# Performance work log

Measured on AMD Instinct MI355X. Metric: run time of the kernel, lower is better.

The kernel has to match this reference:

```python
import math
import jax, jax.numpy as jnp
import numpy as np

H = 768      # hidden_size
NH = 12      # num_attention_heads
K = 3        # attention_num branches (wid = None, 2, 4)
DIV = 5.0    # gauss_divisor = 2**(attention_num-1) + 1
SFT = 1.0    # sft_factor
WIDTHS = (None, 2.0, 4.0)
B, L = 4, 1024


def _layernorm(x, s, b, eps=1e-5):
    m = jnp.mean(x, axis=-1, keepdims=True)
    v = jnp.mean((x - m) ** 2, axis=-1, keepdims=True)
    return (x - m) / jnp.sqrt(v + eps) * s + b


def _log_gauss_bias(props_len, width):
    # matches generate_gauss_weight + log(clamp_min(1e-6))
    center = jnp.arange(props_len, dtype=jnp.float32) / props_len          # (L,)
    wt = jnp.maximum(jnp.float32(width), 0.01) / DIV                       # scalar
    pos = jnp.linspace(0.0, 1.0, props_len)                                # (L,)
    g = (0.3989422804014327 / wt) * jnp.exp(-(pos[None, :] - center[:, None]) ** 2 / (2.0 * wt * wt))
    g = g / jnp.max(g, axis=-1, keepdims=True)
    return jnp.log(jnp.maximum(g, 1e-6))                                   # (L, L)


def _attn(qx, kx, vx, Wq, bq, Wk, bk, Wv, bv, bias, mask):
    Bn, Lq, D = qx.shape
    dh = D // NH
    q = (qx @ Wq + bq).reshape(Bn, Lq, NH, dh)
    k = (kx @ Wk + bk).reshape(Bn, kx.shape[1], NH, dh)
    v = (vx @ Wv + bv).reshape(Bn, vx.shape[1], NH, dh)
    s = jnp.einsum('bqhd,bkhd->bhqk', q, k) / math.sqrt(dh)
    if bias is not None:
        s = s + bias[None, None]                  # cached Gaussian log-bias
    if mask is not None:
        s = s + (1.0 - mask)[:, None, None, :] * (-10000.0)
    p = jax.nn.softmax(s, axis=-1)
    return jnp.einsum('bhqk,bkhd->bqhd', p, v).reshape(Bn, Lq, D)


def _block(x, mask, Wq, bq, Wk, bk, Wv, bv, W1, b1, W2, b2, n1s, n1b, n2s, n2b, bias):
    a = _attn(x, x, x, Wq, bq, Wk, bk, Wv, bv, bias, mask)
    x = _layernorm(x + a, n1s, n1b)
    h = jax.nn.relu(x @ W1 + b1) @ W2 + b2
    return _layernorm(x + h, n2s, n2b)


def setup_inputs():
    key = jax.random.key(0)
    ks = iter(jax.random.split(key, 64))
    def p(*sh):
        return jax.random.normal(next(ks), sh, dtype=jnp.float32) * 0.02
    inp = {}
    inp['input_tensor'] = jax.random.normal(next(ks), (B, L, H), dtype=jnp.float32)
    inp['attention_mask'] = jnp.ones((B, L), dtype=jnp.float32)
    for nm, sh in [('bWq', (K, H, H)), ('bWk', (K, H, H)), ('bWv', (K, H, H)),
                   ('bW1', (K, H, 4 * H)), ('bW2', (K, 4 * H, H)),
                   ('caWq', (H, H)), ('caWk', (H, H)), ('caWv', (H, H)),
                   ('caW1', (H, H)), ('caW2', (H, H)), ('Wl1', (H, H)), ('Wl2', (H, 1))]:
        inp[nm] = p(*sh)
    for nm, sh in [('bbq', (K, H)), ('bbk', (K, H)), ('bbv', (K, H)), ('bb1', (K, 4 * H)), ('bb2', (K, H)),
                   ('cabq', (H,)), ('cabk', (H,)), ('cabv', (H,)), ('cab1', (H,)), ('cab2', (H,)),
                   ('bl1', (H,)), ('bl2', (1,))]:
        inp[nm] = jnp.zeros(sh, dtype=jnp.float32)
    for nm, sh in [('bn1s', (K, H)), ('bn2s', (K, H)), ('bns', (H,)), ('can1s', (H,)), ('can2s', (H,))]:
        inp[nm] = jnp.ones(sh, dtype=jnp.float32)
    for nm, sh in [('bn1b', (K, H)), ('bn2b', (K, H)), ('bnb', (H,)), ('can1b', (H,)), ('can2b', (H,))]:
        inp[nm] = jnp.zeros(sh, dtype=jnp.float32)
    return inp


def reference(input_tensor, attention_mask, bWq, bbq, bWk, bbk, bWv, bbv, bW1, bb1, bW2, bb2,
              bn1s, bn1b, bn2s, bn2b, bns, bnb,
              caWq, cabq, caWk, cabk, caWv, cabv, caW1, cab1, caW2, cab2,
              can1s, can1b, can2s, can2b, Wl1, bl1, Wl2, bl2):
    Bn, Ln, _ = input_tensor.shape
    mask = attention_mask
    biases = [None if w is None else _log_gauss_bias(Ln, w) for w in WIDTHS]
    outs = []
    for i in range(K):
        o = _block(input_tensor, mask,
                   bWq[i], bbq[i], bWk[i], bbk[i], bWv[i], bbv[i],
                   bW1[i], bb1[i], bW2[i], bb2[i],
                   bn1s[i], bn1b[i], bn2s[i], bn2b[i], biases[i])
        outs.append(_layernorm(o, bns, bnb))
    oo = jnp.stack(outs, axis=-1)                                   # (B, L, H, K)
    valid = mask                                                    # (B, L)
    denom = jnp.maximum(valid.sum(axis=1, keepdims=True), 1.0)      # (B, 1)
    mean_token = (oo.mean(-1) * valid[:, :, None]).sum(axis=1, keepdims=True) / denom[:, :, None]  # (B,1,H)
    selected = mean_token  # weight_token=None, mode='global' -> global_token = mean_token
    branch_feat = jnp.transpose(oo, (0, 3, 1, 2)).reshape(Bn * K, Ln, H)
    query_token = jnp.repeat(selected, K, axis=0)                   # (B*K, 1, H)
    branch_mask = jnp.repeat(mask, K, axis=0)                       # (B*K, L)
    # CrossAttention (wid=None, FFN d_ff = H)
    a = _attn(query_token, branch_feat, branch_feat, caWq, cabq, caWk, cabk, caWv, cabv, None, branch_mask)
    q = _layernorm(query_token + a, can1s, can1b)
    t = jax.nn.relu(q @ caW1 + cab1) @ caW2 + cab2
    q = _layernorm(q + t, can2s, can2b)                             # (B*K, 1, H)
    w = q.reshape(Bn, K, H)
    w = jax.nn.relu(w @ Wl1 + bl1)
    w = (w @ Wl2 + bl2)[..., 0]                                     # (B, K)
    w = jax.nn.softmax(w / SFT, axis=-1)
    return (oo * w[:, None, None, :]).sum(axis=-1)                  # (B, L, H)
```

## Files before the change

### kernel.cpp

```cpp
#include <hip/hip_runtime.h>
#include <hip/hip_bf16.h>
#include <cstdint>
#include <cmath>

typedef __hip_bfloat16 bf16;
typedef __attribute__((ext_vector_type(8))) __bf16 bf16x8;
typedef __attribute__((ext_vector_type(4))) float f32x4;

#define NE2C ((size_t)4096 * 768)

__device__ inline float ldv(const void* __restrict__ p, size_t i, bool b){
  return b ? __bfloat162float(((const bf16*)p)[i]) : ((const float*)p)[i];
}

__device__ inline float wave_sum(float v){
  #pragma unroll
  for (int o = 1; o < 64; o <<= 1) v += __shfl_xor(v, o, 64);
  return v;
}
__device__ inline float wave_max(float v){
  #pragma unroll
  for (int o = 1; o < 64; o <<= 1) v = fmaxf(v, __shfl_xor(v, o, 64));
  return v;
}

__device__ __forceinline__ void gload_lds16(const __bf16* g, __bf16* l){
  __builtin_amdgcn_global_load_lds(
      (const __attribute__((address_space(1))) uint32_t*)g,
      (__attribute__((address_space(3))) uint32_t*)l,
      16, 0, 0);
}

__global__ void flag_kernel(const void* __restrict__ bns, int* __restrict__ flagp){
  if (threadIdx.x == 0) flagp[0] = (((const uint32_t*)bns)[0] == 0x3F800000u) ? 0 : 1;
}

__global__ __launch_bounds__(256) void cvtb_kernel(const void* __restrict__ in, __bf16* __restrict__ out,
                                                   int n, const int* __restrict__ flagp){
  const bool isb = flagp[0] != 0;
  int i = blockIdx.x * 256 + threadIdx.x;
  if (i < n) out[i] = (__bf16)ldv(in, i, isb);
}

__global__ __launch_bounds__(256) void transpose_kernel(const void* __restrict__ in, size_t in_off, size_t in_zstride,
    __bf16* __restrict__ out, size_t out_off, size_t out_zstride, int K, int N, const int* __restrict__ flagp)
{
  const bool isb = flagp[0] != 0;
  const int z = blockIdx.z;
  const size_t ioff = in_off + (size_t)z * in_zstride;
  __bf16* op = out + out_off + (size_t)z * out_zstride;
  const int n0 = blockIdx.x * 64, k0 = blockIdx.y * 64;
  __shared__ __bf16 T[64][65];
  const int cr = threadIdx.x >> 6, cc = threadIdx.x & 63;
  #pragma unroll
  for (int it = 0; it < 16; ++it) {
    int r = it * 4 + cr;
    T[r][cc] = (__bf16)ldv(in, ioff + (size_t)(k0 + r) * N + (n0 + cc), isb);
  }
  __syncthreads();
  #pragma unroll
  for (int it = 0; it < 16; ++it) {
    int r = it * 4 + cr;
    op[(size_t)(n0 + r) * K + (k0 + cc)] = T[cc][r];
  }
}

__global__ __launch_bounds__(256) void biaspack_kernel(const void* bbq, const void* bbk, const void* bbv,
    const void* bb1, const void* bb2, const void* cabk, const void* cabv,
    float* __restrict__ pool, const int* __restrict__ flagp)
{
  const bool isb = flagp[0] != 0;
  int idx = blockIdx.x * 256 + threadIdx.x;
  if (idx >= 19968) return;
  float v;
  if (idx < 6912) {
    int i = idx / 2304, rem = idx % 2304;
    int m = rem / 768, c = rem % 768;
    const void* src = (m == 0) ? bbq : ((m == 1) ? bbk : bbv);
    v = ldv(src, (size_t)i * 768 + c, isb);
  } else if (idx < 16128) v = ldv(bb1, idx - 6912, isb);
  else if (idx < 18432)   v = ldv(bb2, idx - 16128, isb);
  else if (idx < 19200)   v = ldv(cabk, idx - 18432, isb);
  else                    v = ldv(cabv, idx - 19200, isb);
  pool[idx] = v;
}

__global__ __launch_bounds__(256) void gaussbias_kernel(float* __restrict__ gb)
{
  const int br = blockIdx.x >> 10;
  const int q  = blockIdx.x & 1023;
  const float inv2wt2 = (br == 0) ? 3.125f : 0.78125f;
  const float c2 = inv2wt2 * 1.4426950408889634f;
  const float cq = (float)q * (1.f / 1024.f);
  const float kst = roundf(cq * 1023.f);
  const float dd = kst * (1.f / 1023.f) - cq;
  const float dmin = dd * dd;
  float* row = gb + (size_t)br * 1048576 + (size_t)q * 1024;
  for (int j = threadIdx.x; j < 1024; j += 256) {
    float d2 = (float)j * (1.f / 1023.f) - cq;
    row[j] = fmaxf((dmin - d2 * d2) * c2, -19.9315686f);
  }
}

__global__ __launch_bounds__(256) void gemm_mfma_kernel(
    const __bf16* __restrict__ A, size_t a_zstride,
    const __bf16* __restrict__ WT, const float* __restrict__ biasp,
    __bf16* __restrict__ C, int M, int N, int K, int relu)
{
  const int z = blockIdx.z;
  A  += (size_t)z * a_zstride;
  WT += (size_t)z * (size_t)N * K;
  biasp += (size_t)z * N;
  C  += (size_t)z * (size_t)M * N;
  const int m0 = blockIdx.y * 128, n0 = blockIdx.x * 128;
  const int tid = threadIdx.x, w = tid >> 6, lane = tid & 63;
  const int quad = lane >> 4, r16 = lane & 15;
  const int wr = w >> 1, wc = w & 1;
  __shared__ __align__(16) __bf16 As[128 * 32];
  __shared__ __align__(16) __bf16 Bs[128 * 32];
  f32x4 acc[4][4];
  #pragma unroll
  for (int i = 0; i < 4; ++i)
    #pragma unroll
    for (int j = 0; j < 4; ++j) acc[i][j] = (f32x4){0.f, 0.f, 0.f, 0.f};

  const int srow = tid >> 2;
  const int scc  = (tid & 3) * 8;

  for (int k0 = 0; k0 < K; k0 += 32) {
    __syncthreads();
    #pragma unroll
    for (int it = 0; it < 2; ++it) {
      int row = it * 64 + srow;
      const __bf16* gA = A  + (size_t)(m0 + row) * K + k0 + scc;
      const __bf16* gB = WT + (size_t)(n0 + row) * K + k0 + scc;
      __bf16* lA = &As[(it * 256 + w * 64) * 8];
      __bf16* lB = &Bs[(it * 256 + w * 64) * 8];
      gload_lds16(gA, lA);
      gload_lds16(gB, lB);
    }
    __syncthreads();
    bf16x8 af[4], bf[4];
    #pragma unroll
    for (int mt = 0; mt < 4; ++mt) af[mt] = *(const bf16x8*)&As[(wr * 64 + mt * 16 + r16) * 32 + quad * 8];
    #pragma unroll
    for (int nt = 0; nt < 4; ++nt) bf[nt] = *(const bf16x8*)&Bs[(wc * 64 + nt * 16 + r16) * 32 + quad * 8];
    #pragma unroll
    for (int mt = 0; mt < 4; ++mt)
      #pragma unroll
      for (int nt = 0; nt < 4; ++nt)
        acc[mt][nt] = __builtin_amdgcn_mfma_f32_16x16x32_bf16(af[mt], bf[nt], acc[mt][nt], 0, 0, 0);
  }
  #pragma unroll
  for (int nt = 0; nt < 4; ++nt) {
    int col = n0 + wc * 64 + nt * 16 + r16;
    float bv = biasp[col];
    #pragma unroll
    for (int mt = 0; mt < 4; ++mt) {
      int rowb = m0 + wr * 64 + mt * 16 + quad * 4;
      #pragma unroll
      for (int reg = 0; reg < 4; ++reg) {
        float v = acc[mt][nt][reg] + bv;
        if (relu) v = fmaxf(v, 0.f);
        C[(size_t)(rowb + reg) * N + col] = (__bf16)v;
      }
    }
  }
}

__global__ __launch_bounds__(256) void gemm_small_kernel(const float* __restrict__ A, const void* __restrict__ W,
    size_t woff, const void* __restrict__ bias, size_t boff, float* __restrict__ C,
    int N, int K, int relu, const int* __restrict__ flagp)
{
  const bool isb = flagp[0] != 0;
  const int row = blockIdx.y;
  const int c = blockIdx.x * 64 + (threadIdx.x & 63);
  const int ks = threadIdx.x >> 6;
  const int klen = K >> 2;
  const float* ar = A + (size_t)row * K + ks * klen;
  const size_t wbase = woff + (size_t)ks * klen * N + c;
  float acc = 0.f;
  #pragma unroll 4
  for (int k = 0; k < klen; ++k)
    acc += ar[k] * ldv(W, wbase + (size_t)k * N, isb);
  __shared__ float red[4][64];
  red[ks][threadIdx.x & 63] = acc;
  __syncthreads();
  if (threadIdx.x < 64) {
    float v = red[0][threadIdx.x] + red[1][threadIdx.x] + red[2][threadIdx.x] + red[3][threadIdx.x];
    v += ldv(bias, boff + c, isb);
    if (relu) v = fmaxf(v, 0.f);
    C[(size_t)row * N + c] = v;
  }
}

__global__ __launch_bounds__(256) void attn_mfma_kernel(
    const __bf16* __restrict__ QKV, const void* __restrict__ mask,
    const float* __restrict__ gbias,
    __bf16* __restrict__ Aout, const int* __restrict__ flagp)
{
  const bool isb = flagp[0] != 0;
  const int bz = blockIdx.z;
  const int b = bz & 3, br = bz >> 2;
  const __bf16* Q  = QKV + (size_t)br * 3 * NE2C;
  const __bf16* Kg = Q + NE2C;
  const __bf16* Vg = Q + 2 * NE2C;
  Aout += (size_t)br * NE2C;
  const int has_bias = br > 0;

  const int h = blockIdx.y;
  const int tid = threadIdx.x;
  const int w = tid >> 6, lane = tid & 63;
  const int quad = lane >> 4, r16 = lane & 15;
  const int qbase = blockIdx.x * 64 + w * 16;

  __shared__ __align__(16) __bf16 Ks[64 * 72];
  __shared__ __align__(16) __bf16 Vt[64 * 72];
  __shared__ __align__(16) __bf16 Ps[4][16 * 72];

  const __bf16* qrow = Q + ((size_t)(b * 1024 + qbase + r16)) * 768 + h * 64;
  bf16x8 aq0 = *(const bf16x8*)(qrow + quad * 8);
  bf16x8 aq1 = *(const bf16x8*)(qrow + 32 + quad * 8);

  const float* brow[4];
  if (has_bias) {
    const float* gb = gbias + (size_t)(br - 1) * 1048576 + r16;
    #pragma unroll
    for (int reg = 0; reg < 4; ++reg)
      brow[reg] = gb + (size_t)(qbase + quad * 4 + reg) * 1024;
  }

  float m_r[4], l_r[4];
  f32x4 O[4];
  #pragma unroll
  for (int n = 0; n < 4; ++n) O[n] = (f32x4){0.f, 0.f, 0.f, 0.f};
  #pragma unroll
  for (int reg = 0; reg < 4; ++reg) { m_r[reg] = -1e30f; l_r[reg] = 0.f; }

  const int dd = tid & 63;
  const int rb = tid >> 6;
  const int dswz = (dd >> 3) & 7;

  const int kr_row0 = tid >> 3;
  const int kr_c8   = (tid & 7) * 8;
  const size_t kcol  = (size_t)h * 64 + kr_c8;
  const size_t vcol  = (size_t)h * 64 + dd;
  const size_t bbase = (size_t)b * 1024;

  const float SCL = 0.18033688f;
  const float MBIG = 14426.9504f;
  const float THR2 = 11.5415603f;

  bf16x8 kpre0, kpre1;
  bf16x8 vpre0, vpre1;

  {
    kpre0 = *(const bf16x8*)(Kg + (bbase + kr_row0)      * 768 + kcol);
    kpre1 = *(const bf16x8*)(Kg + (bbase + kr_row0 + 32) * 768 + kcol);
    const int r0 = rb * 16;
    #pragma unroll
    for (int i = 0; i < 8; ++i) {
      vpre0[i] = Vg[(bbase + r0 + i)     * 768 + vcol];
      vpre1[i] = Vg[(bbase + r0 + 8 + i) * 768 + vcol];
    }
  }

  for (int c0 = 0; c0 < 1024; c0 += 64) {
    __syncthreads();
    *(bf16x8*)&Ks[kr_row0 * 72 + kr_c8]        = kpre0;
    *(bf16x8*)&Ks[(kr_row0 + 32) * 72 + kr_c8] = kpre1;
    {
      int blk0 = ((rb * 16)     >> 3) ^ dswz;
      int blk1 = ((rb * 16 + 8) >> 3) ^ dswz;
      *(bf16x8*)&Vt[dd * 72 + blk0 * 8] = vpre0;
      *(bf16x8*)&Vt[dd * 72 + blk1 * 8] = vpre1;
    }
    __syncthreads();

    if (c0 + 64 < 1024) {
      const size_t cb = bbase + c0 + 64;
      kpre0 = *(const bf16x8*)(Kg + (cb + kr_row0)      * 768 + kcol);
      kpre1 = *(const bf16x8*)(Kg + (cb + kr_row0 + 32) * 768 + kcol);
      const int r0 = rb * 16;
      #pragma unroll
      for (int i = 0; i < 8; ++i) {
        vpre0[i] = Vg[(cb + r0 + i)     * 768 + vcol];
        vpre1[i] = Vg[(cb + r0 + 8 + i) * 768 + vcol];
      }
    }

    float s4[4][4], p4[4][4];
    #pragma unroll
    for (int t = 0; t < 4; ++t) {
      bf16x8 b0 = *(const bf16x8*)&Ks[(t * 16 + r16) * 72 + quad * 8];
      bf16x8 b1 = *(const bf16x8*)&Ks[(t * 16 + r16) * 72 + 32 + quad * 8];
      f32x4 accq = (f32x4){0.f, 0.f, 0.f, 0.f};
      accq = __builtin_amdgcn_mfma_f32_16x16x32_bf16(aq0, b0, accq, 0, 0, 0);
      accq = __builtin_amdgcn_mfma_f32_16x16x32_bf16(aq1, b1, accq, 0, 0, 0);
      int kk = c0 + t * 16 + r16;
      float mk = ldv(mask, (size_t)(b * 1024 + kk), isb);
      float mterm = fmaf(mk, MBIG, -MBIG);
      if (has_bias) {
        #pragma unroll
        for (int reg = 0; reg < 4; ++reg)
          s4[t][reg] = fmaf(accq[reg], SCL, mterm) + brow[reg][c0 + t * 16];
      } else {
        #pragma unroll
        for (int reg = 0; reg < 4; ++reg)
          s4[t][reg] = fmaf(accq[reg], SCL, mterm);
      }
    }
    float tm[4];
    #pragma unroll
    for (int reg = 0; reg < 4; ++reg) {
      float t0 = fmaxf(fmaxf(s4[0][reg], s4[1][reg]), fmaxf(s4[2][reg], s4[3][reg]));
      #pragma unroll
      for (int off = 1; off < 16; off <<= 1) t0 = fmaxf(t0, __shfl_xor(t0, off, 64));
      tm[reg] = t0;
    }
    bool nosc = (tm[0] - m_r[0] <= THR2) && (tm[1] - m_r[1] <= THR2)
             && (tm[2] - m_r[2] <= THR2) && (tm[3] - m_r[3] <= THR2);
    if (!__all(nosc)) {
      #pragma unroll
      for (int reg = 0; reg < 4; ++reg) {
        float mnew = fmaxf(m_r[reg], tm[reg]);
        float alpha = exp2f(m_r[reg] - mnew);
        l_r[reg] *= alpha;
        m_r[reg] = mnew;
        #pragma unroll
        for (int n = 0; n < 4; ++n) O[n][reg] *= alpha;
      }
    }
    #pragma unroll
    for (int reg = 0; reg < 4; ++reg) {
      float rs = 0.f;
      #pragma unroll
      for (int t = 0; t < 4; ++t) { float p = exp2f(s4[t][reg] - m_r[reg]); p4[t][reg] = p; rs += p; }
      l_r[reg] += rs;
    }
    __bf16* pw = &Ps[w][0];
    #pragma unroll
    for (int t = 0; t < 4; ++t)
      #pragma unroll
      for (int reg = 0; reg < 4; ++reg)
        pw[(quad * 4 + reg) * 72 + t * 16 + r16] = (__bf16)p4[t][reg];
    bf16x8 ap0 = *(const bf16x8*)&pw[r16 * 72 + quad * 8];
    bf16x8 ap1 = *(const bf16x8*)&pw[r16 * 72 + 32 + quad * 8];
    __builtin_amdgcn_s_setprio(1);
    #pragma unroll
    for (int n = 0; n < 4; ++n) {
      int dr = n * 16 + r16;
      int sw = (dr >> 3) & 7;
      bf16x8 bv0 = *(const bf16x8*)&Vt[dr * 72 + (quad ^ sw) * 8];
      bf16x8 bv1 = *(const bf16x8*)&Vt[dr * 72 + ((quad + 4) ^ sw) * 8];
      O[n] = __builtin_amdgcn_mfma_f32_16x16x32_bf16(ap0, bv0, O[n], 0, 0, 0);
      O[n] = __builtin_amdgcn_mfma_f32_16x16x32_bf16(ap1, bv1, O[n], 0, 0, 0);
    }
    __builtin_amdgcn_s_setprio(0);
  }
  #pragma unroll
  for (int reg = 0; reg < 4; ++reg) {
    float lv = l_r[reg];
    #pragma unroll
    for (int off = 1; off < 16; off <<= 1) lv += __shfl_xor(lv, off, 64);
    l_r[reg] = lv;
  }
  #pragma unroll
  for (int n = 0; n < 4; ++n)
    #pragma unroll
    for (int reg = 0; reg < 4; ++reg) {
      int qg = qbase + quad * 4 + reg;
      Aout[((size_t)(b * 1024 + qg)) * 768 + h * 64 + n * 16 + r16] = (__bf16)(O[n][reg] / l_r[reg]);
    }
}

__global__ __launch_bounds__(256) void lnb_b_kernel(const __bf16* __restrict__ x, const __bf16* __restrict__ a,
    const void* __restrict__ sc, const void* __restrict__ bi, __bf16* __restrict__ out,
    const int* __restrict__ flagp)
{
  const bool isb = flagp[0] != 0;
  const int br = blockIdx.y;
  a   += (size_t)br * NE2C;
  out += (size_t)br * NE2C;
  const size_t so = (size_t)br * 768;
  int r = blockIdx.x;
  const __bf16* xr = x + (size_t)r * 768;
  const __bf16* ar = a + (size_t)r * 768;
  int t = threadIdx.x;
  float v[3]; float s = 0.f, ss = 0.f;
  #pragma unroll
  for (int j = 0; j < 3; j++) {
    int c = t + j * 256;
    float val = (float)xr[c] + (float)ar[c];
    v[j] = val; s += val; ss += val * val;
  }
  s = wave_sum(s); ss = wave_sum(ss);
  __shared__ float sred[8];
  __shared__ float stats[2];
  int lane = t & 63, wid = t >> 6;
  if (lane == 0) { sred[wid] = s; sred[4 + wid] = ss; }
  __syncthreads();
  if (t == 0) {
    float S = sred[0] + sred[1] + sred[2] + sred[3];
    float SS = sred[4] + sred[5] + sred[6] + sred[7];
    float mean = S * (1.f / 768.f);
    float var = fmaxf(SS * (1.f / 768.f) - mean * mean, 0.f);
    stats[0] = mean; stats[1] = rsqrtf(var + 1e-5f);
  }
  __syncthreads();
  float mean = stats[0], rstd = stats[1];
  #pragma unroll
  for (int j = 0; j < 3; j++) {
    int c = t + j * 256;
    out[(size_t)r * 768 + c] = (__bf16)((v[j] - mean) * rstd * ldv(sc, so + c, isb) + ldv(bi, so + c, isb));
  }
}

__global__ __launch_bounds__(256) void lnb2_b_kernel(const __bf16* __restrict__ x, const __bf16* __restrict__ a,
    const void* __restrict__ sc1, const void* __restrict__ bi1,
    const void* __restrict__ sc2, const void* __restrict__ bi2,
    __bf16* __restrict__ out, const int* __restrict__ flagp)
{
  const bool isb = flagp[0] != 0;
  const int br = blockIdx.y;
  x   += (size_t)br * NE2C;
  a   += (size_t)br * NE2C;
  out += (size_t)br * NE2C;
  const size_t s1off = (size_t)br * 768;
  int r = blockIdx.x;
  const __bf16* xr = x + (size_t)r * 768;
  const __bf16* ar = a + (size_t)r * 768;
  int t = threadIdx.x;
  int lane = t & 63, wid = t >> 6;
  __shared__ float sred[8], stats[2], sred2[8], stats2[2];

  float v[3]; float s = 0.f, ss = 0.f;
  #pragma unroll
  for (int j = 0; j < 3; j++) {
    int c = t + j * 256;
    float val = (float)xr[c] + (float)ar[c];
    v[j] = val; s += val; ss += val * val;
  }
  s = wave_sum(s); ss = wave_sum(ss);
  if (lane == 0) { sred[wid] = s; sred[4 + wid] = ss; }
  __syncthreads();
  if (t == 0) {
    float S = sred[0] + sred[1] + sred[2] + sred[3];
    float SS = sred[4] + sred[5] + sred[6] + sred[7];
    float mean = S * (1.f / 768.f);
    float var = fmaxf(SS * (1.f / 768.f) - mean * mean, 0.f);
    stats[0] = mean; stats[1] = rsqrtf(var + 1e-5f);
  }
  __syncthreads();
  float mean = stats[0], rstd = stats[1];
  float y[3]; float s2 = 0.f, ss2 = 0.f;
  #pragma unroll
  for (int j = 0; j < 3; j++) {
    int c = t + j * 256;
    float yv = (v[j] - mean) * rstd * ldv(sc1, s1off + c, isb) + ldv(bi1, s1off + c, isb);
    yv = (float)(__bf16)yv;
    y[j] = yv; s2 += yv; ss2 += yv * yv;
  }
  s2 = wave_sum(s2); ss2 = wave_sum(ss2);
  if (lane == 0) { sred2[wid] = s2; sred2[4 + wid] = ss2; }
  __syncthreads();
  if (t == 0) {
    float S = sred2[0] + sred2[1] + sred2[2] + sred2[3];
    float SS = sred2[4] + sred2[5] + sred2[6] + sred2[7];
    float mean2 = S * (1.f / 768.f);
    float var2 = fmaxf(SS * (1.f / 768.f) - mean2 * mean2, 0.f);
    stats2[0] = mean2; stats2[1] = rsqrtf(var2 + 1e-5f);
  }
  __syncthreads();
  float mean2 = stats2[0], rstd2 = stats2[1];
  #pragma unroll
  for (int j = 0; j < 3; j++) {
    int c = t + j * 256;
    out[(size_t)r * 768 + c] = (__bf16)((y[j] - mean2) * rstd2 * ldv(sc2, c, isb) + ldv(bi2, c, isb));
  }
}

__global__ __launch_bounds__(256) void ln_kernel(const float* __restrict__ x, const float* __restrict__ a,
    const void* __restrict__ sc, size_t soff, const void* __restrict__ bi, size_t boff,
    float* __restrict__ out, int xdiv, const int* __restrict__ flagp)
{
  const bool isb = flagp[0] != 0;
  int r = blockIdx.x;
  const float* xr = x + (size_t)(xdiv > 1 ? r / xdiv : r) * 768;
  const float* ar = a ? a + (size_t)r * 768 : nullptr;
  int t = threadIdx.x;
  float v[3]; float s = 0.f, ss = 0.f;
  #pragma unroll
  for (int j = 0; j < 3; j++) {
    int c = t + j * 256;
    float val = xr[c] + (ar ? ar[c] : 0.f);
    v[j] = val; s += val; ss += val * val;
  }
  s = wave_sum(s); ss = wave_sum(ss);
  __shared__ float sred[8];
  __shared__ float stats[2];
  int lane = t & 63, wid = t >> 6;
  if (lane == 0) { sred[wid] = s; sred[4 + wid] = ss; }
  __syncthreads();
  if (t == 0) {
    float S = sred[0] + sred[1] + sred[2] + sred[3];
    float SS = sred[4] + sred[5] + sred[6] + sred[7];
    float mean = S * (1.f / 768.f);
    float var = fmaxf(SS * (1.f / 768.f) - mean * mean, 0.f);
    stats[0] = mean; stats[1] = rsqrtf(var + 1e-5f);
  }
  __syncthreads();
  float mean = stats[0], rstd = stats[1];
  #pragma unroll
  for (int j = 0; j < 3; j++) {
    int c = t + j * 256;
    out[(size_t)r * 768 + c] = (v[j] - mean) * rstd * ldv(sc, soff + c, isb) + ldv(bi, boff + c, isb);
  }
}

__global__ __launch_bounds__(256) void meantok_part_kernel(const __bf16* __restrict__ OO, const void* __restrict__ mask,
    float* __restrict__ partials, const int* __restrict__ flagp)
{
  const bool isb = flagp[0] != 0;
  const size_t NE = NE2C;
  int h = blockIdx.x * 256 + threadIdx.x;
  int b = blockIdx.y, lc = blockIdx.z;
  const __bf16* base = OO + (size_t)(b * 1024 + lc * 64) * 768 + h;
  float acc = 0.f;
  for (int l = 0; l < 64; ++l) {
    float mk = ldv(mask, (size_t)(b * 1024 + lc * 64 + l), isb);
    size_t off = (size_t)l * 768;
    acc += mk * ((float)base[off] + (float)base[off + NE] + (float)base[off + 2 * NE]);
  }
  partials[((size_t)(b * 16 + lc)) * 768 + h] = acc;
}

__global__ __launch_bounds__(256) void meantok_fin_kernel(const float* __restrict__ partials,
    const void* __restrict__ mask, float* __restrict__ mt, const int* __restrict__ flagp)
{
  const bool isb = flagp[0] != 0;
  int h = blockIdx.x * 256 + threadIdx.x;
  int b = blockIdx.y;
  int t = threadIdx.x;
  float ms = 0.f;
  for (int j = t; j < 1024; j += 256) ms += ldv(mask, (size_t)(b * 1024 + j), isb);
  ms = wave_sum(ms);
  __shared__ float sred[4];
  __shared__ float msume;
  if ((t & 63) == 0) sred[t >> 6] = ms;
  __syncthreads();
  if (t == 0) msume = fmaxf(sred[0] + sred[1] + sred[2] + sred[3], 1.f);
  __syncthreads();
  float acc = 0.f;
  #pragma unroll
  for (int lc = 0; lc < 16; ++lc) acc += partials[((size_t)(b * 16 + lc)) * 768 + h];
  mt[b * 768 + h] = acc * (1.f / 3.f) / msume;
}

__global__ __launch_bounds__(64) void crossattn_kernel(const float* __restrict__ qC, const __bf16* __restrict__ kC,
    const __bf16* __restrict__ vC, const void* __restrict__ mask, float* __restrict__ caout,
    const int* __restrict__ flagp)
{
  const bool isb = flagp[0] != 0;
  int h = blockIdx.x, i = blockIdx.y, b = blockIdx.z;
  int lane = threadIdx.x;
  __shared__ float sbuf[1024];
  __shared__ float qsh[64];
  qsh[lane] = qC[b * 768 + h * 64 + lane];
  const size_t rowbase = (size_t)(i * 4 + b) * 1024;
  const __bf16* kb = kC + rowbase * 768 + h * 64;
  float lmax = -1e30f;
  for (int j = lane; j < 1024; j += 64) {
    const __bf16* kr = kb + (size_t)j * 768;
    float s = 0.f;
    #pragma unroll
    for (int d = 0; d < 64; d++) s += qsh[d] * (float)kr[d];
    s *= 0.125f;
    float mk = ldv(mask, (size_t)(b * 1024 + j), isb);
    s += (1.0f - mk) * (-10000.0f);
    sbuf[j] = s;
    lmax = fmaxf(lmax, s);
  }
  float mm = wave_max(lmax);
  float lsum = 0.f;
  for (int j = lane; j < 1024; j += 64) {
    float p = __expf(sbuf[j] - mm);
    sbuf[j] = p;
    lsum += p;
  }
  lsum = wave_sum(lsum);
  const __bf16* vb = vC + rowbase * 768 + h * 64;
  float acc = 0.f;
  for (int j = 0; j < 1024; j++) acc += sbuf[j] * (float)vb[(size_t)j * 768 + lane];
  caout[(size_t)(b * 3 + i) * 768 + h * 64 + lane] = acc / lsum;
}

__global__ __launch_bounds__(256) void logits_kernel(const float* __restrict__ wfeat, const void* __restrict__ Wl2,
    const void* __restrict__ bl2, float* __restrict__ logits, const int* __restrict__ flagp)
{
  const bool isb = flagp[0] != 0;
  int r = blockIdx.x, t = threadIdx.x;
  float s = 0.f;
  #pragma unroll
  for (int j = 0; j < 3; j++) {
    int c = t + j * 256;
    s += wfeat[(size_t)r * 768 + c] * ldv(Wl2, c, isb);
  }
  s = wave_sum(s);
  __shared__ float sred[4];
  if ((t & 63) == 0) sred[t >> 6] = s;
  __syncthreads();
  if (t == 0) logits[r] = sred[0] + sred[1] + sred[2] + sred[3] + ldv(bl2, 0, isb);
}

__global__ void wsoftmax_kernel(const float* __restrict__ logits, float* __restrict__ w)
{
  int b = threadIdx.x;
  if (b < 4) {
    float l0 = logits[b * 3], l1 = logits[b * 3 + 1], l2 = logits[b * 3 + 2];
    float m = fmaxf(l0, fmaxf(l1, l2));
    float e0 = __expf(l0 - m), e1 = __expf(l1 - m), e2 = __expf(l2 - m);
    float inv = 1.f / (e0 + e1 + e2);
    w[b * 3] = e0 * inv; w[b * 3 + 1] = e1 * inv; w[b * 3 + 2] = e2 * inv;
  }
}

__global__ __launch_bounds__(256) void combine_kernel(const __bf16* __restrict__ OO, const float* __restrict__ w,
                                                      void* __restrict__ out, const int* __restrict__ flagp)
{
  const bool isb = flagp[0] != 0;
  const size_t NE = NE2C;
  size_t idx = (size_t)blockIdx.x * 256 + threadIdx.x;
  int b = (int)(idx / (1024 * 768));
  float w0 = w[b * 3], w1 = w[b * 3 + 1], w2 = w[b * 3 + 2];
  float v = (float)OO[idx] * w0 + (float)OO[idx + NE] * w1 + (float)OO[idx + 2 * NE] * w2;
  if (isb) ((bf16*)out)[idx] = __float2bfloat16(v);
  else     ((float*)out)[idx] = v;
}

extern "C" void kernel_launch(void* const* d_in, const int* in_sizes, int n_in,
                              void* d_out, int out_size, void* d_ws, size_t ws_size,
                              hipStream_t stream)
{
  const void* X    = d_in[0];
  const void* mask = d_in[1];
  const void* bWq  = d_in[2];
  const void* bWk  = d_in[3];
  const void* bWv  = d_in[4];
  const void* bW1  = d_in[5];
  const void* bW2  = d_in[6];
  const void* caWq = d_in[7];
  const void* caWk = d_in[8];
  const void* caWv = d_in[9];
  const void* caW1 = d_in[10];
  const void* caW2 = d_in[11];
  const void* Wl1  = d_in[12];
  const void* Wl2  = d_in[13];
  const void* bbq  = d_in[14];
  const void* bbk  = d_in[15];
  const void* bbv  = d_in[16];
  const void* bb1  = d_in[17];
  const void* bb2  = d_in[18];
  const void* cabq = d_in[19];
  const void* cabk = d_in[20];
  const void* cabv = d_in[21];
  const void* cab1 = d_in[22];
  const void* cab2 = d_in[23];
  const void* bl1  = d_in[24];
  const void* bl2  = d_in[25];
  const void* bn1s = d_in[26];
  const void* bn2s = d_in[27];
  const void* bns  = d_in[28];
  const void* can1s= d_in[29];
  const void* can2s= d_in[30];
  const void* bn1b = d_in[31];
  const void* bn2b = d_in[32];
  const void* bnb  = d_in[33];
  const void* can1b= d_in[34];
  const void* can2b= d_in[35];

  const size_t NE2 = NE2C;
  const size_t WSQ = (size_t)768 * 768;
  const size_t WSF = (size_t)768 * 3072;

  __bf16* XFb  = (__bf16*)d_ws;
  __bf16* Rb   = XFb + NE2;
  __bf16* X1   = Rb + 12 * NE2;
  __bf16* AF2  = X1 + 3 * NE2;
  __bf16* WTqkv= AF2 + 3 * NE2;
  __bf16* WT1  = WTqkv + 9 * WSQ;
  __bf16* WT2  = WT1 + 3 * WSF;
  __bf16* WTc  = WT2 + 3 * WSF;
  float*  pool = (float*)(WTc + 2 * WSQ);
  float*  mt     = pool + 19968;
  float*  qC     = mt + 3072;
  float*  caout  = qC + 3072;
  float*  q1     = caout + 9216;
  float*  t1     = q1 + 9216;
  float*  t2     = t1 + 9216;
  float*  q2     = t2 + 9216;
  float*  wfeat  = q2 + 9216;
  float*  logits = wfeat + 9216;
  float*  wsm    = logits + 16;
  int*    flagp  = (int*)(wsm + 16);
  float*  partials = (float*)(flagp + 64);
  __bf16* OO = X1;
  __bf16* kC = Rb;
  __bf16* vC = Rb + 3 * NE2;
  float*  gb = (float*)X1;

  dim3 blk256(256);
  flag_kernel<<<dim3(1), dim3(64), 0, stream>>>(bns, flagp);
  cvtb_kernel<<<dim3((int)((NE2 + 255) / 256)), blk256, 0, stream>>>(X, XFb, (int)NE2, flagp);

  transpose_kernel<<<dim3(12, 12, 3), blk256, 0, stream>>>(bWq, 0, WSQ, WTqkv, 0 * WSQ, 3 * WSQ, 768, 768, flagp);
  transpose_kernel<<<dim3(12, 12, 3), blk256, 0, stream>>>(bWk, 0, WSQ, WTqkv, 1 * WSQ, 3 * WSQ, 768, 768, flagp);
  transpose_kernel<<<dim3(12, 12, 3), blk256, 0, stream>>>(bWv, 0, WSQ, WTqkv, 2 * WSQ, 3 * WSQ, 768, 768, flagp);
  transpose_kernel<<<dim3(48, 12, 3), blk256, 0, stream>>>(bW1, 0, WSF, WT1, 0, WSF, 768, 3072, flagp);
  transpose_kernel<<<dim3(12, 48, 3), blk256, 0, stream>>>(bW2, 0, WSF, WT2, 0, WSF, 3072, 768, flagp);
  transpose_kernel<<<dim3(12, 12, 1), blk256, 0, stream>>>(caWk, 0, 0, WTc, 0, 0, 768, 768, flagp);
  transpose_kernel<<<dim3(12, 12, 1), blk256, 0, stream>>>(caWv, 0, 0, WTc, WSQ, 0, 768, 768, flagp);
  biaspack_kernel<<<dim3(78), blk256, 0, stream>>>(bbq, bbk, bbv, bb1, bb2, cabk, cabv, pool, flagp);
  gaussbias_kernel<<<dim3(2048), blk256, 0, stream>>>(gb);

  gemm_mfma_kernel<<<dim3(6, 32, 9), blk256, 0, stream>>>(XFb, 0, WTqkv, pool, Rb, 4096, 768, 768, 0);
  attn_mfma_kernel<<<dim3(16, 12, 12), blk256, 0, stream>>>(Rb, mask, gb, AF2, flagp);
  lnb_b_kernel<<<dim3(4096, 3), blk256, 0, stream>>>(XFb, AF2, bn1s, bn1b, X1, flagp);
  gemm_mfma_kernel<<<dim3(24, 32, 3), blk256, 0, stream>>>(X1, NE2, WT1, pool + 6912, Rb, 4096, 3072, 768, 1);
  gemm_mfma_kernel<<<dim3(6, 32, 3), blk256, 0, stream>>>(Rb, 4 * NE2, WT2, pool + 16128, AF2, 4096, 768, 3072, 0);
  lnb2_b_kernel<<<dim3(4096, 3), blk256, 0, stream>>>(X1, AF2, bn2s, bn2b, bns, bnb, OO, flagp);

  meantok_part_kernel<<<dim3(3, 4, 16), blk256, 0, stream>>>(OO, mask, partials, flagp);
  meantok_fin_kernel<<<dim3(3, 4), blk256, 0, stream>>>(partials, mask, mt, flagp);
  gemm_small_kernel<<<dim3(12, 4), blk256, 0, stream>>>(mt, caWq, 0, cabq, 0, qC, 768, 768, 0, flagp);
  gemm_mfma_kernel<<<dim3(6, 96, 2), blk256, 0, stream>>>(OO, 0, WTc, pool + 18432, kC, 12288, 768, 768, 0);
  crossattn_kernel<<<dim3(12, 3, 4), dim3(64), 0, stream>>>(qC, kC, vC, mask, caout, flagp);
  ln_kernel<<<dim3(12), blk256, 0, stream>>>(mt, caout, can1s, 0, can1b, 0, q1, 3, flagp);
  gemm_small_kernel<<<dim3(12, 12), blk256, 0, stream>>>(q1, caW1, 0, cab1, 0, t1, 768, 768, 1, flagp);
  gemm_small_kernel<<<dim3(12, 12), blk256, 0, stream>>>(t1, caW2, 0, cab2, 0, t2, 768, 768, 0, flagp);
  ln_kernel<<<dim3(12), blk256, 0, stream>>>(q1, t2, can2s, 0, can2b, 0, q2, 1, flagp);
  gemm_small_kernel<<<dim3(12, 12), blk256, 0, stream>>>(q2, Wl1, 0, bl1, 0, wfeat, 768, 768, 1, flagp);
  logits_kernel<<<dim3(12), blk256, 0, stream>>>(wfeat, Wl2, bl2, logits, flagp);
  wsoftmax_kernel<<<dim3(1), dim3(64), 0, stream>>>(logits, wsm);
  combine_kernel<<<dim3((int)(NE2 / 256)), blk256, 0, stream>>>(OO, wsm, d_out, flagp);
}
```

Baseline: 991.1 us.

## Permute gauss bias layout for vector loads, skip all-ones mask, widen crossattn

The Gaussian bias table is now written in a permuted column order, so each lane in the attention kernel fetches its four bias values with one 16-byte load instead of four scalar loads. A new single-block kernel checks on the device whether the mask is all ones and sets a flag; the attention and cross-attention kernels then skip the per-key mask loads. The online-softmax rescale check now uses per-lane maxima and only does the shuffle reduction when some lane exceeds the threshold. The cross-attention kernel moves from 64 to 256 threads, with vectorized key loads and block-level reductions. The mask check is computed at run time, so other masks still take the full path, at the cost of one extra tiny launch.

```diff
diff --git a/kernel.cpp b/kernel.cpp
--- a/kernel.cpp
+++ b/kernel.cpp
@@ -33,6 +33,19 @@
 
 __global__ void flag_kernel(const void* __restrict__ bns, int* __restrict__ flagp){
   if (threadIdx.x == 0) flagp[0] = (((const uint32_t*)bns)[0] == 0x3F800000u) ? 0 : 1;
+}
+
+__global__ __launch_bounds__(256) void maskchk_kernel(const void* __restrict__ mask, int* __restrict__ flagp){
+  const bool isb = flagp[0] != 0;
+  int t = threadIdx.x;
+  int ok = 1;
+  for (int j = t; j < 4096; j += 256) ok &= (ldv(mask, (size_t)j, isb) == 1.0f) ? 1 : 0;
+  __shared__ int allok;
+  if (t == 0) allok = 1;
+  __syncthreads();
+  if (!ok) atomicAnd(&allok, 0);
+  __syncthreads();
+  if (t == 0) flagp[1] = allok;
 }
 
 __global__ __launch_bounds__(256) void cvtb_kernel(const void* __restrict__ in, __bf16* __restrict__ out,
@@ -96,9 +109,11 @@
   const float dd = kst * (1.f / 1023.f) - cq;
   const float dmin = dd * dd;
   float* row = gb + (size_t)br * 1048576 + (size_t)q * 1024;
-  for (int j = threadIdx.x; j < 1024; j += 256) {
-    float d2 = (float)j * (1.f / 1023.f) - cq;
-    row[j] = fmaxf((dmin - d2 * d2) * c2, -19.9315686f);
+  for (int o = threadIdx.x; o < 1024; o += 256) {
+    int cb = o >> 6, rem = o & 63, rr = rem >> 2, t = rem & 3;
+    int k = cb * 64 + t * 16 + rr;
+    float d2 = (float)k * (1.f / 1023.f) - cq;
+    row[o] = fmaxf((dmin - d2 * d2) * c2, -19.9315686f);
   }
 }
 
@@ -200,6 +215,7 @@
     __bf16* __restrict__ Aout, const int* __restrict__ flagp)
 {
   const bool isb = flagp[0] != 0;
+  const bool mall = flagp[1] != 0;
   const int bz = blockIdx.z;
   const int b = bz & 3, br = bz >> 2;
   const __bf16* Q  = QKV + (size_t)br * 3 * NE2C;
@@ -222,12 +238,12 @@
   bf16x8 aq0 = *(const bf16x8*)(qrow + quad * 8);
   bf16x8 aq1 = *(const bf16x8*)(qrow + 32 + quad * 8);
 
-  const float* brow[4];
+  const float* bq4[4];
   if (has_bias) {
-    const float* gb = gbias + (size_t)(br - 1) * 1048576 + r16;
+    const float* gbb = gbias + (size_t)(br - 1) * 1048576 + r16 * 4;
     #pragma unroll
     for (int reg = 0; reg < 4; ++reg)
-      brow[reg] = gb + (size_t)(qbase + quad * 4 + reg) * 1024;
+      bq4[reg] = gbb + (size_t)(qbase + quad * 4 + reg) * 1024;
   }
 
   float m_r[4], l_r[4];
@@ -289,6 +305,12 @@
       }
     }
 
+    f32x4 bv4[4];
+    if (has_bias) {
+      #pragma unroll
+      for (int reg = 0; reg < 4; ++reg) bv4[reg] = *(const f32x4*)(bq4[reg] + c0);
+    }
+
     float s4[4][4], p4[4][4];
     #pragma unroll
     for (int t = 0; t < 4; ++t) {
@@ -297,33 +319,35 @@
       f32x4 accq = (f32x4){0.f, 0.f, 0.f, 0.f};
       accq = __builtin_amdgcn_mfma_f32_16x16x32_bf16(aq0, b0, accq, 0, 0, 0);
       accq = __builtin_amdgcn_mfma_f32_16x16x32_bf16(aq1, b1, accq, 0, 0, 0);
-      int kk = c0 + t * 16 + r16;
-      float mk = ldv(mask, (size_t)(b * 1024 + kk), isb);
-      float mterm = fmaf(mk, MBIG, -MBIG);
+      float mterm = 0.f;
+      if (!mall) {
+        int kk = c0 + t * 16 + r16;
+        float mk = ldv(mask, (size_t)(b * 1024 + kk), isb);
+        mterm = fmaf(mk, MBIG, -MBIG);
+      }
       if (has_bias) {
         #pragma unroll
         for (int reg = 0; reg < 4; ++reg)
-          s4[t][reg] = fmaf(accq[reg], SCL, mterm) + brow[reg][c0 + t * 16];
+          s4[t][reg] = fmaf(accq[reg], SCL, mterm) + bv4[reg][t];
       } else {
         #pragma unroll
         for (int reg = 0; reg < 4; ++reg)
           s4[t][reg] = fmaf(accq[reg], SCL, mterm);
       }
     }
-    float tm[4];
-    #pragma unroll
-    for (int reg = 0; reg < 4; ++reg) {
-      float t0 = fmaxf(fmaxf(s4[0][reg], s4[1][reg]), fmaxf(s4[2][reg], s4[3][reg]));
-      #pragma unroll
-      for (int off = 1; off < 16; off <<= 1) t0 = fmaxf(t0, __shfl_xor(t0, off, 64));
-      tm[reg] = t0;
-    }
-    bool nosc = (tm[0] - m_r[0] <= THR2) && (tm[1] - m_r[1] <= THR2)
-             && (tm[2] - m_r[2] <= THR2) && (tm[3] - m_r[3] <= THR2);
-    if (!__all(nosc)) {
+    float mlane[4];
+    #pragma unroll
+    for (int reg = 0; reg < 4; ++reg)
+      mlane[reg] = fmaxf(fmaxf(s4[0][reg], s4[1][reg]), fmaxf(s4[2][reg], s4[3][reg]));
+    bool need = (mlane[0] > m_r[0] + THR2) || (mlane[1] > m_r[1] + THR2)
+             || (mlane[2] > m_r[2] + THR2) || (mlane[3] > m_r[3] + THR2);
+    if (__any(need)) {
       #pragma unroll
       for (int reg = 0; reg < 4; ++reg) {
-        float mnew = fmaxf(m_r[reg], tm[reg]);
+        float t0 = mlane[reg];
+        #pragma unroll
+        for (int off = 1; off < 16; off <<= 1) t0 = fmaxf(t0, __shfl_xor(t0, off, 64));
+        float mnew = fmaxf(m_r[reg], t0);
         float alpha = exp2f(m_r[reg] - mnew);
         l_r[reg] *= alpha;
         m_r[reg] = mnew;
@@ -557,42 +581,64 @@
   mt[b * 768 + h] = acc * (1.f / 3.f) / msume;
 }
 
-__global__ __launch_bounds__(64) void crossattn_kernel(const float* __restrict__ qC, const __bf16* __restrict__ kC,
+__global__ __launch_bounds__(256) void crossattn_kernel(const float* __restrict__ qC, const __bf16* __restrict__ kC,
     const __bf16* __restrict__ vC, const void* __restrict__ mask, float* __restrict__ caout,
     const int* __restrict__ flagp)
 {
   const bool isb = flagp[0] != 0;
+  const bool mall = flagp[1] != 0;
   int h = blockIdx.x, i = blockIdx.y, b = blockIdx.z;
-  int lane = threadIdx.x;
+  int tid = threadIdx.x, lane = tid & 63, wv = tid >> 6;
   __shared__ float sbuf[1024];
   __shared__ float qsh[64];
-  qsh[lane] = qC[b * 768 + h * 64 + lane];
+  __shared__ float red[8];
+  __shared__ float vred[4][64];
+  if (tid < 64) qsh[tid] = qC[b * 768 + h * 64 + tid];
+  __syncthreads();
   const size_t rowbase = (size_t)(i * 4 + b) * 1024;
   const __bf16* kb = kC + rowbase * 768 + h * 64;
   float lmax = -1e30f;
-  for (int j = lane; j < 1024; j += 64) {
+  for (int j = tid; j < 1024; j += 256) {
     const __bf16* kr = kb + (size_t)j * 768;
     float s = 0.f;
     #pragma unroll
-    for (int d = 0; d < 64; d++) s += qsh[d] * (float)kr[d];
+    for (int d0 = 0; d0 < 8; ++d0) {
+      bf16x8 kv = *(const bf16x8*)(kr + d0 * 8);
+      #pragma unroll
+      for (int e = 0; e < 8; ++e) s += qsh[d0 * 8 + e] * (float)kv[e];
+    }
     s *= 0.125f;
-    float mk = ldv(mask, (size_t)(b * 1024 + j), isb);
-    s += (1.0f - mk) * (-10000.0f);
+    if (!mall) {
+      float mk = ldv(mask, (size_t)(b * 1024 + j), isb);
+      s += (1.0f - mk) * (-10000.0f);
+    }
     sbuf[j] = s;
     lmax = fmaxf(lmax, s);
   }
-  float mm = wave_max(lmax);
+  lmax = wave_max(lmax);
+  if (lane == 0) red[wv] = lmax;
+  __syncthreads();
+  float mm = fmaxf(fmaxf(red[0], red[1]), fmaxf(red[2], red[3]));
   float lsum = 0.f;
-  for (int j = lane; j < 1024; j += 64) {
+  for (int j = tid; j < 1024; j += 256) {
     float p = __expf(sbuf[j] - mm);
     sbuf[j] = p;
     lsum += p;
   }
   lsum = wave_sum(lsum);
+  if (lane == 0) red[4 + wv] = lsum;
+  __syncthreads();
+  float L = red[4] + red[5] + red[6] + red[7];
   const __bf16* vb = vC + rowbase * 768 + h * 64;
   float acc = 0.f;
-  for (int j = 0; j < 1024; j++) acc += sbuf[j] * (float)vb[(size_t)j * 768 + lane];
-  caout[(size_t)(b * 3 + i) * 768 + h * 64 + lane] = acc / lsum;
+  for (int j = wv * 256; j < wv * 256 + 256; ++j)
+    acc += sbuf[j] * (float)vb[(size_t)j * 768 + lane];
+  vred[wv][lane] = acc;
+  __syncthreads();
+  if (tid < 64) {
+    float a = vred[0][tid] + vred[1][tid] + vred[2][tid] + vred[3][tid];
+    caout[(size_t)(b * 3 + i) * 768 + h * 64 + tid] = a / L;
+  }
 }
 
 __global__ __launch_bounds__(256) void logits_kernel(const float* __restrict__ wfeat, const void* __restrict__ Wl2,
@@ -711,6 +757,7 @@
 
   dim3 blk256(256);
   flag_kernel<<<dim3(1), dim3(64), 0, stream>>>(bns, flagp);
+  maskchk_kernel<<<dim3(1), blk256, 0, stream>>>(mask, flagp);
   cvtb_kernel<<<dim3((int)((NE2 + 255) / 256)), blk256, 0, stream>>>(X, XFb, (int)NE2, flagp);
 
   transpose_kernel<<<dim3(12, 12, 3), blk256, 0, stream>>>(bWq, 0, WSQ, WTqkv, 0 * WSQ, 3 * WSQ, 768, 768, flagp);
@@ -734,7 +781,7 @@
   meantok_fin_kernel<<<dim3(3, 4), blk256, 0, stream>>>(partials, mask, mt, flagp);
   gemm_small_kernel<<<dim3(12, 4), blk256, 0, stream>>>(mt, caWq, 0, cabq, 0, qC, 768, 768, 0, flagp);
   gemm_mfma_kernel<<<dim3(6, 96, 2), blk256, 0, stream>>>(OO, 0, WTc, pool + 18432, kC, 12288, 768, 768, 0);
-  crossattn_kernel<<<dim3(12, 3, 4), dim3(64), 0, stream>>>(qC, kC, vC, mask, caout, flagp);
+  crossattn_kernel<<<dim3(12, 3, 4), blk256, 0, stream>>>(qC, kC, vC, mask, caout, flagp);
   ln_kernel<<<dim3(12), blk256, 0, stream>>>(mt, caout, can1s, 0, can1b, 0, q1, 3, flagp);
   gemm_small_kernel<<<dim3(12, 12), blk256, 0, stream>>>(q1, caW1, 0, cab1, 0, t1, 768, 768, 1, flagp);
   gemm_small_kernel<<<dim3(12, 12), blk256, 0, stream>>>(t1, caW2, 0, cab2, 0, t2, 768, 768, 0, flagp);
```

New measurement: 933.9 us. 5.8% less time.
